# Performance work log

Measured on AMD Instinct MI355X. Metric: run time of the kernel, lower is better.

The kernel has to match this reference:

```python
import jax, jax.numpy as jnp
import numpy as np

B, N, DIM = 4, 1024, 1024
H, DH, ORDER = 16, 64, 3
MAXREL = 64
INNER = H * DH
VOCAB = 2 * MAXREL + 1
SCALE = DH ** -0.5
TOPK = int(0.25 * N)  # topk_ratio=0.25 default when top_k is None


def setup_inputs() -> dict:
    key = jax.random.key(0)
    ks = jax.random.split(key, 8)
    s = 0.02
    return {
        "x": jax.random.normal(ks[0], (B, N, DIM), jnp.float32),
        "Wqkv": jax.random.normal(ks[1], (3 * INNER, DIM), jnp.float32) * s,
        "bqkv": jnp.zeros((3 * INNER,), jnp.float32),
        "Wout": jax.random.normal(ks[2], (DIM, INNER), jnp.float32) * s,
        "bout": jnp.zeros((DIM,), jnp.float32),
        "rel_k_emb": jax.random.normal(ks[3], (VOCAB, DH), jnp.float32) * s,
        "rel_v_emb": jax.random.normal(ks[4], (VOCAB, DH), jnp.float32) * s,
        "alphas_raw": jax.random.normal(ks[5], (ORDER, H), jnp.float32) * 0.5,
    }


def reference(x, Wqkv, bqkv, Wout, bout, rel_k_emb, rel_v_emb, alphas_raw):
    b, n, _ = x.shape
    qkv = x @ Wqkv.T + bqkv  # [b, n, 3*inner]
    q, k, v = jnp.split(qkv, 3, axis=-1)
    to_heads = lambda t: t.reshape(b, n, H, DH).transpose(0, 2, 1, 3)  # b h n d
    q, k, v = to_heads(q), to_heads(k), to_heads(v)

    scores = jnp.einsum('bhid,bhjd->bhij', q, k) * SCALE

    # relative position bias on keys
    coords = jnp.arange(n)
    dist = jnp.clip(coords[:, None] - coords[None, :], -MAXREL, MAXREL) + MAXREL  # [n, n]
    rel_k = rel_k_emb[dist]  # [n, n, d]
    scores = scores + jnp.einsum('bhid,ijd->bhij', q, rel_k)

    # top-k thresholding per query row
    top_vals = jax.lax.top_k(scores, TOPK)[0]
    threshold = top_vals[..., -1:]
    scores = jnp.where(scores < threshold, -jnp.inf, scores)

    attn = jax.nn.softmax(scores, axis=-1)  # [b, h, n, n]

    rel_v = rel_v_emb[dist]  # [n, n, d]
    alphas = jax.nn.sigmoid(alphas_raw)  # [order, h]

    # monomial-basis polynomial filter: res = sum_i alpha_i * A^(i+1) V (+ relV term at i=0)
    res = jnp.zeros_like(v)
    v_curr = v
    for i in range(ORDER):
        a_v = jnp.einsum('bhij,bhjd->bhid', attn, v_curr)
        if i == 0:
            a_v = a_v + jnp.einsum('bhij,ijd->bhid', attn, rel_v)
        v_curr = a_v
        res = res + alphas[i][None, :, None, None] * v_curr

    out = res.transpose(0, 2, 1, 3).reshape(b, n, INNER)
    return out @ Wout.T + bout
```

## Files before the change

kernel.cpp:

```cpp
#include <hip/hip_runtime.h>

typedef unsigned short u16;
typedef unsigned int   u32;
typedef unsigned long long u64;
typedef __bf16 bf16x8 __attribute__((ext_vector_type(8)));
typedef float  floatx4 __attribute__((ext_vector_type(4)));

#define DEV static __device__ __forceinline__

DEV u16 f2bf(float f){ u32 x = __float_as_uint(f); return (u16)((x + 0x7fffu + ((x>>16)&1u)) >> 16); }
DEV float bf2f(u16 h){ return __uint_as_float(((u32)h)<<16); }
DEV u32 cvt_pk_bf16(float a, float b){ u32 r; asm("v_cvt_pk_bf16_f32 %0, %1, %2" : "=v"(r) : "v"(a), "v"(b)); return r; }

DEV void load_lds16(const u16* g, u16* l){
  __builtin_amdgcn_global_load_lds((const __attribute__((address_space(1))) u32*)g,
                                   (__attribute__((address_space(3))) u32*)l, 16, 0, 0);
}

DEV void barrier_fenced(){
  asm volatile("" ::: "memory");
  __builtin_amdgcn_sched_barrier(0);
  __builtin_amdgcn_s_barrier();
  __builtin_amdgcn_sched_barrier(0);
  asm volatile("" ::: "memory");
}

DEV u32 unswz64(u32 p){
  u32 r0 = ((p>>6) ^ (p>>8)) & 1u;
  u32 b4 = ((p>>4) & 1u) ^ r0;
  u32 b5 = ((p>>5) ^ (p>>7)) & 1u;
  return (p & ~0x70u) | (b4<<4) | (b5<<5) | (r0<<6);
}
DEV bf16x8 ldfrag(const u16* base, int row, int lane){
  u32 off = ((u32)row<<6) + (((u32)lane>>4)<<4);
  off ^= (u32)(row&7)<<4;
  return *(const bf16x8*)((const char*)base + off);
}

template<int BM, int BN>
__global__ __launch_bounds__(512, 4) void gemm8(
    const u16* __restrict__ A, const u16* __restrict__ Bm, float* __restrict__ C,
    const float* __restrict__ bias, int K, int lda, int ldb, int ldc, int ncmax)
{
  constexpr int MT = (BM/2)/16;
  constexpr int NT = (BN/4)/16;
  constexpr int AU = BM*32;
  constexpr int BU = BN*32;
  constexpr int STRIDE = AU + BU;
  __shared__ u16 smem[4*STRIDE];

  const int tid = threadIdx.x, wid = tid>>6, lane = tid&63;
  const int m0 = blockIdx.y * BM, n0 = blockIdx.x * BN;

  const u32 g = unswz64((u32)tid*16);
  const int srow = g>>6, schunk = (g&63)>>1;
  const u16* ga0 = A  + (long long)(m0 + srow)*lda + schunk;
  const u16* gb0 = Bm + (long long)(n0 + srow)*ldb + schunk;

  u16* lA0 = smem + (wid<<9);
  u16* lB0 = smem + AU + (wid<<9);

  const int wm = wid>>2, wn = wid&3;
  const int lr = lane&15, lq = lane>>4;

  auto stage = [&](int s){
    const int c = s & 3;
    if (BM == 128 || wid < 4) load_lds16(ga0 + (s<<5), lA0 + c*STRIDE);
    load_lds16(gb0 + (s<<5), lB0 + c*STRIDE);
  };

  floatx4 acc[MT][NT] = {};
  const int nk = K >> 5;

#define G_STEP(CC, VA, VB) do { \
    if (BM == 128 || wid < 4) asm volatile("s_waitcnt vmcnt(" VA ")" ::: "memory"); \
    else                      asm volatile("s_waitcnt vmcnt(" VB ")" ::: "memory"); \
    barrier_fenced(); \
    const u16* Asc = smem + (u32)(CC)*STRIDE; \
    const u16* Bsc = Asc + AU; \
    bf16x8 af[MT]; \
    _Pragma("unroll") \
    for (int mt=0; mt<MT; ++mt) af[mt] = ldfrag(Asc, wm*(BM/2) + mt*16 + lr, lane); \
    _Pragma("unroll") \
    for (int nt=0; nt<NT; ++nt) { \
      bf16x8 bfr = ldfrag(Bsc, wn*(BN/4) + nt*16 + lr, lane); \
      _Pragma("unroll") \
      for (int mt=0; mt<MT; ++mt) \
        acc[mt][nt] = __builtin_amdgcn_mfma_f32_16x16x32_bf16(af[mt], bfr, acc[mt][nt], 0, 0, 0); \
    } \
    barrier_fenced(); \
  } while(0)

#pragma unroll
  for (int p = 0; p < 4; ++p) stage(p);

  for (int s = 0; s < nk - 4; ++s){
    G_STEP(s & 3, "6", "3");
    stage(s + 4);
  }
  G_STEP((nk-4) & 3, "6", "3");
  G_STEP((nk-3) & 3, "4", "2");
  G_STEP((nk-2) & 3, "2", "1");
  G_STEP((nk-1) & 3, "0", "0");
#undef G_STEP

#pragma unroll
  for (int nt=0; nt<NT; ++nt) {
    const int col = n0 + wn*(BN/4) + nt*16 + lr;
    if (col < ncmax) {
      const float bv = bias ? bias[col] : 0.f;
#pragma unroll
      for (int mt=0; mt<MT; ++mt) {
#pragma unroll
        for (int r=0; r<4; ++r) {
          const int row = m0 + wm*(BM/2) + mt*16 + lq*4 + r;
          C[(long long)row*ldc + col] = acc[mt][nt][r] + bv;
        }
      }
    }
  }
}

__global__ __launch_bounds__(512, 4) void av8(
    const u16* __restrict__ P,
    const u16* __restrict__ V,
    u16* __restrict__ vout,
    float* __restrict__ resb,
    const float* __restrict__ araw, int K, int order, int accum, int wv)
{
  __shared__ u16 smem[32768];
  const int tid = threadIdx.x, wid = tid>>6, lane = tid&63;
  const int L = blockIdx.x;
  const int z  = (L & 7) + ((L >> 7) << 3);
  const int m0 = ((L >> 3) & 15) * 64;
  const int lr = lane&15, lq = lane>>4;

  const int sw = wid & 3;
  const u32 g = unswz64((u32)(sw*1024 + lane*16));
  const int srow = g>>6, schunk = (g&63)>>1;
  const u16* gsrc = (wid < 4)
      ? P + (long long)z*1212416 + (long long)(m0 + srow)*1184 + schunk
      : V + (long long)z*75776   + (long long)srow*1184 + schunk;
  const int bsel = (wid < 4) ? 0 : 2048;
  u16* ldst0 = smem + bsel + (sw<<9);

  const int wm = wid>>2, wn = wid&3;
  const int wm32 = wm*32, wn16 = wn*16;
  const int nk = K >> 5;

  auto stage = [&](int p){ load_lds16(gsrc + (p<<5), ldst0 + ((p&7)<<12)); };

  floatx4 acc[2] = {};

#define AV_STEP(CC, VC) do { \
    asm volatile("s_waitcnt vmcnt(" VC ")" ::: "memory"); \
    barrier_fenced(); \
    const u16* Asc = smem + ((u32)(CC)<<12); \
    const u16* Bsc = Asc + 2048; \
    bf16x8 bfr = ldfrag(Bsc, wn16 + lr, lane); \
    bf16x8 af0 = ldfrag(Asc, wm32 + lr, lane); \
    bf16x8 af1 = ldfrag(Asc, wm32 + 16 + lr, lane); \
    acc[0] = __builtin_amdgcn_mfma_f32_16x16x32_bf16(af0, bfr, acc[0], 0, 0, 0); \
    acc[1] = __builtin_amdgcn_mfma_f32_16x16x32_bf16(af1, bfr, acc[1], 0, 0, 0); \
    barrier_fenced(); \
  } while(0)

#pragma unroll
  for (int p = 0; p < 8; ++p) stage(p);

  for (int s = 0; s < nk - 8; ++s){
    AV_STEP(s & 7, "7");
    stage(s + 8);
  }
  AV_STEP((nk-8) & 7, "7");
  AV_STEP((nk-7) & 7, "6");
  AV_STEP((nk-6) & 7, "5");
  AV_STEP((nk-5) & 7, "4");
  AV_STEP((nk-4) & 7, "3");
  AV_STEP((nk-3) & 7, "2");
  AV_STEP((nk-2) & 7, "1");
  AV_STEP((nk-1) & 7, "0");
#undef AV_STEP

  const int h = z & 15;
  const float alpha = 1.f/(1.f + __expf(-araw[order*16 + h]));
  float* rb = resb + (long long)z * 65536;
  const int d = wn16 + lr;
  __syncthreads();
#pragma unroll
  for (int mt=0; mt<2; ++mt){
#pragma unroll
    for (int r=0; r<4; ++r){
      const int row = wm32 + mt*16 + lq*4 + r;
      const float v = acc[mt][r];
      const long long ri = (long long)(m0+row)*64 + d;
      rb[ri] = accum ? (rb[ri] + alpha*v) : (alpha*v);
      smem[d*136 + row] = f2bf(v);
    }
  }
  __syncthreads();
  if (wv){
    const int dd = tid>>3, cc = (tid&7)*8;
    u16* vp = vout + (long long)z*75776 + (long long)dd*1184 + m0 + cc;
    const u16* sp = smem + dd*136 + cc;
    uint4 uu;
    uu.x = sp[0] | ((u32)sp[1]<<16);
    uu.y = sp[2] | ((u32)sp[3]<<16);
    uu.z = sp[4] | ((u32)sp[5]<<16);
    uu.w = sp[6] | ((u32)sp[7]<<16);
    *(uint4*)(vp) = uu;
  }
}

__global__ __launch_bounds__(1024, 8) void score_topk(
    const u16* __restrict__ qF,
    const u16* __restrict__ kxF,
    u16* __restrict__ P)
{
  constexpr int SROW = 1156;
  __shared__ float sm[16*SROW];
  const int tid = threadIdx.x, wid = tid>>6, lane = tid&63;
  const int L = blockIdx.x;
  const int z  = (L & 7) + ((L >> 9) << 3);
  const int mt = (L >> 3) & 63;
  const int m0 = mt*16;
  const int lr = lane&15, lq = lane>>4;

  const u16* Aq = qF + (((long long)z*64 + mt)*6*64 + lane)*8;
  const u16* Bq = kxF + ((long long)z*80*6*64 + lane)*8;

  bf16x8 af[6];
#pragma unroll
  for (int kc=0;kc<6;++kc) af[kc] = *(const bf16x8*)(Aq + kc*512);

  const int base = wid*5;
  {
    floatx4 acc[5];
#pragma unroll
    for (int t=0;t<5;++t) acc[t] = floatx4{0.f,0.f,0.f,0.f};
#pragma unroll
    for (int t=0;t<5;++t){
      if (base + t < 73){
        const u16* bp = Bq + (long long)(base+t)*3072;
        bf16x8 b0 = *(const bf16x8*)(bp);
        bf16x8 b1 = *(const bf16x8*)(bp + 512);
        bf16x8 b2 = *(const bf16x8*)(bp + 1024);
        bf16x8 b3 = *(const bf16x8*)(bp + 1536);
        bf16x8 b4 = *(const bf16x8*)(bp + 2048);
        bf16x8 b5 = *(const bf16x8*)(bp + 2560);
        acc[t] = __builtin_amdgcn_mfma_f32_16x16x32_bf16(af[0], b0, acc[t], 0, 0, 0);
        acc[t] = __builtin_amdgcn_mfma_f32_16x16x32_bf16(af[1], b1, acc[t], 0, 0, 0);
        acc[t] = __builtin_amdgcn_mfma_f32_16x16x32_bf16(af[2], b2, acc[t], 0, 0, 0);
        acc[t] = __builtin_amdgcn_mfma_f32_16x16x32_bf16(af[3], b3, acc[t], 0, 0, 0);
        acc[t] = __builtin_amdgcn_mfma_f32_16x16x32_bf16(af[4], b4, acc[t], 0, 0, 0);
        acc[t] = __builtin_amdgcn_mfma_f32_16x16x32_bf16(af[5], b5, acc[t], 0, 0, 0);
      }
    }
#pragma unroll
    for (int t=0;t<5;++t){
      if (base + t < 73){
        const int col = (base+t)*16 + lr;
        if (col < 1153){
#pragma unroll
          for (int r=0;r<4;++r) sm[(lq*4+r)*SROW + col] = acc[t][r];
        }
      }
    }
  }
  __syncthreads();

  {
    const int row = wid;
    const int i = m0 + row;
    float* R = sm + row*SROW;

    float v[16];
#pragma unroll
    for (int x=0;x<8;++x){
      float2 f = *(const float2*)(R + x*128 + lane*2);
      v[2*x] = f.x; v[2*x+1] = f.y;
    }
#pragma unroll
    for (int x=0;x<16;++x){
      const int j = (x>>1)*128 + lane*2 + (x&1);
      int dl = i - j; dl = dl > 64 ? 64 : (dl < -64 ? -64 : dl);
      v[x] += R[1024 + dl + 64];
    }
    u32 u[16];
#pragma unroll
    for (int x=0;x<16;++x){
      u32 bb = __float_as_uint(v[x]);
      u[x] = bb ^ ((u32)((int)bb >> 31) | 0x80000000u);
    }
    u32 thr = 0;
#pragma unroll 1
    for (int bit=31; bit>=0; --bit){
      const u32 cand = thr | (1u<<bit);
      int c = 0;
#pragma unroll
      for (int x=0;x<16;++x) c += __popcll(__ballot(u[x] >= cand));
      if (c == 256){
        u32 mn = 0xFFFFFFFFu;
#pragma unroll
        for (int x=0;x<16;++x) if (u[x] >= cand && u[x] < mn) mn = u[x];
        for (int o=32;o;o>>=1){ u32 t = __shfl_xor(mn, o); mn = t < mn ? t : mn; }
        thr = mn;
        break;
      }
      if (c > 256) thr = cand;
    }
    float m = -3.0e38f;
#pragma unroll
    for (int x=0;x<16;++x) m = fmaxf(m, v[x]);
    for (int o=32;o;o>>=1) m = fmaxf(m, __shfl_xor(m, o));
    float e[16]; float Z = 0.f;
#pragma unroll
    for (int x=0;x<16;++x){
      e[x] = (u[x] >= thr) ? __expf(v[x]-m) : 0.f;
      Z += e[x];
    }
    for (int o=32;o;o>>=1) Z += __shfl_xor(Z, o);
    const float rz = 1.f / Z;

    u16* Pr = P + ((long long)z*1024 + i)*1184;
    u32* Pr32 = (u32*)Pr;
    float s0 = 0.f, s1 = 0.f;
#pragma unroll
    for (int x=0;x<8;++x){
      const float p0 = e[2*x]*rz, p1 = e[2*x+1]*rz;
      *(float2*)(R + x*128 + lane*2) = float2{p0, p1};
      Pr32[x*64 + lane] = cvt_pk_bf16(p0, p1);
      const int j0 = x*128 + lane*2;
      if (j0     >= i+64) s0 += p0;
      if (j0     <= i-64) s1 += p0;
      if (j0 + 1 >= i+64) s0 += p1;
      if (j0 + 1 <= i-64) s1 += p1;
    }
    for (int o=32;o;o>>=1){ s0 += __shfl_xor(s0,o); s1 += __shfl_xor(s1,o); }
    {
      const int t = lane + 1;
      const int j = i + 64 - t;
      const float wv = (j>=0 && j<1024) ? R[j] : 0.f;
      Pr[1024 + t] = f2bf(wv);
      if (lane < 63){
        const int t2 = lane + 65;
        const int j2 = i + 64 - t2;
        const float wv2 = (j2>=0 && j2<1024) ? R[j2] : 0.f;
        Pr[1024 + t2] = f2bf(wv2);
      }
      if (lane == 0){ Pr[1024] = f2bf(s0); Pr[1152] = f2bf(s1); }
      if (lane >= 33) Pr[1120 + lane] = 0;
    }
  }
}

__global__ __launch_bounds__(256) void planeize(const float* __restrict__ src, u16* __restrict__ dst,
                                                int total, int modeB){
  int idx = blockIdx.x*256 + threadIdx.x;
  if (idx >= total) return;
  int c = idx & 1023, r = idx >> 10;
  float v = src[idx];
  u16 hi = f2bf(v); u16 lo = f2bf(v - bf2f(hi));
  u16* d = dst + (long long)r*3072 + c;
  if (modeB){ d[0]=hi; d[1024]=hi; d[2048]=lo; }
  else      { d[0]=hi; d[1024]=lo; d[2048]=hi; }
}

__global__ __launch_bounds__(256) void build_qk(const float* __restrict__ qkv,
                                                u16* __restrict__ qF, u16* __restrict__ kxF){
  int idx = blockIdx.x*256 + threadIdx.x;
  int d = idx & 63, n = (idx>>6) & 1023, bh = idx >> 16;
  int b = bh >> 4, h = bh & 15;
  long long src = (long long)(b*1024 + n)*3072 + h*64 + d;
  float qv = qkv[src];
  float kv = qkv[src + 1024] * 0.125f;
  u16 qhi=f2bf(qv), qlo=f2bf(qv - bf2f(qhi));
  u16 khi=f2bf(kv), klo=f2bf(kv - bf2f(khi));
  const int lane = (n&15) + (((d&31)>>3)<<4);
  const int elem = d&7, kc0 = d>>5;
  u16* q = qF + ((((long long)bh*64 + (n>>4))*6*64) + lane)*8 + elem;
  q[(kc0+0)*512] = qhi; q[(kc0+2)*512] = qlo; q[(kc0+4)*512] = qhi;
  u16* kx = kxF + ((((long long)bh*80 + (n>>4))*6*64) + lane)*8 + elem;
  kx[(kc0+0)*512] = khi; kx[(kc0+2)*512] = khi; kx[(kc0+4)*512] = klo;
}

__global__ __launch_bounds__(256) void build_kxrel(const float* __restrict__ relk, u16* __restrict__ kxF){
  int idx = blockIdx.x*256 + threadIdx.x;
  int d = idx & 63, t = (idx>>6) & 255, bh = idx >> 14;
  u16 hi=0, lo=0;
  if (t < 129){ float v = relk[t*64 + d]; hi = f2bf(v); lo = f2bf(v - bf2f(hi)); }
  const int nrow = 1024 + t;
  const int lane = (t&15) + (((d&31)>>3)<<4);
  const int elem = d&7, kc0 = d>>5;
  u16* kx = kxF + ((((long long)bh*80 + (nrow>>4))*6*64) + lane)*8 + elem;
  kx[(kc0+0)*512] = hi; kx[(kc0+2)*512] = hi; kx[(kc0+4)*512] = lo;
}

__global__ __launch_bounds__(256) void build_vT(const float* __restrict__ qkv, u16* __restrict__ vA){
  __shared__ float tb[64][65];
  int bh = blockIdx.x >> 4, ntile = blockIdx.x & 15;
  int b = bh >> 4, h = bh & 15;
  int tid = threadIdx.x;
  int nl = tid >> 2, dc = (tid & 3)*16;
  const float* sp = qkv + (long long)(b*1024 + ntile*64 + nl)*3072 + 2048 + h*64 + dc;
#pragma unroll
  for (int j=0;j<16;j+=4){
    float4 f = *(const float4*)(sp + j);
    tb[dc+j+0][nl]=f.x; tb[dc+j+1][nl]=f.y; tb[dc+j+2][nl]=f.z; tb[dc+j+3][nl]=f.w;
  }
  __syncthreads();
  int d = tid >> 2, nc = (tid & 3)*16;
  u16* dp = vA + ((long long)bh*64 + d)*1184 + ntile*64 + nc;
#pragma unroll
  for (int j=0;j<16;j+=8){
    u16 a0=f2bf(tb[d][nc+j+0]), a1=f2bf(tb[d][nc+j+1]), a2=f2bf(tb[d][nc+j+2]), a3=f2bf(tb[d][nc+j+3]);
    u16 a4=f2bf(tb[d][nc+j+4]), a5=f2bf(tb[d][nc+j+5]), a6=f2bf(tb[d][nc+j+6]), a7=f2bf(tb[d][nc+j+7]);
    uint4 uu; uu.x=a0|((u32)a1<<16); uu.y=a2|((u32)a3<<16); uu.z=a4|((u32)a5<<16); uu.w=a6|((u32)a7<<16);
    *(uint4*)(dp + j) = uu;
  }
}

__global__ __launch_bounds__(256) void build_vText(const float* __restrict__ relv, u16* __restrict__ vA){
  int idx = blockIdx.x*256 + threadIdx.x;
  int t = idx % 160; int rest = idx / 160; int d = rest & 63; int bh = rest >> 6;
  u16 hv = 0;
  if (t < 129) hv = f2bf(relv[t*64 + d]);
  vA[((long long)bh*64 + d)*1184 + 1024 + t] = hv;
}

__global__ __launch_bounds__(256) void build_resS(const float* __restrict__ res, u16* __restrict__ resS){
  int idx = blockIdx.x*256 + threadIdx.x;
  int d = idx & 63, n = (idx>>6) & 1023, bh = idx >> 16;
  int b = bh >> 4, h = bh & 15;
  float v = res[idx];
  u16 hi = f2bf(v), lo = f2bf(v - bf2f(hi));
  u16* p = resS + (long long)(b*1024 + n)*3072 + h*64 + d;
  p[0]=hi; p[1024]=lo; p[2048]=hi;
}

extern "C" void kernel_launch(void* const* d_in, const int* in_sizes, int n_in,
                              void* d_out, int out_size, void* d_ws, size_t ws_size,
                              hipStream_t stream) {
  const float* x    = (const float*)d_in[0];
  const float* Wqkv = (const float*)d_in[1];
  const float* bqkv = (const float*)d_in[2];
  const float* Wout = (const float*)d_in[3];
  const float* bout = (const float*)d_in[4];
  const float* relk = (const float*)d_in[5];
  const float* relv = (const float*)d_in[6];
  const float* araw = (const float*)d_in[7];
  float* out = (float*)d_out;

  char* w = (char*)d_ws;
  size_t off = 0;
  auto take = [&](size_t bytes)->char*{ char* p = w + off; off += (bytes + 255) & ~(size_t)255; return p; };

  char* regionA = take(94371840);
  u16*   xS    = (u16*)  (regionA);
  u16*   wqS   = (u16*)  (regionA + 25165824);
  float* qkv32 = (float*)(regionA + 44040192);
  u16*   Ph    = (u16*)  (regionA);
  u16*   resS  = (u16*)  (regionA);
  u16*   woS   = (u16*)  (regionA + 25165824);
  u16*   qF    = (u16*)take(25165824);
  u16*   kxF   = (u16*)take(31457280);
  u16*   vA    = (u16*)take(9699328);
  u16*   vB    = (u16*)take(9699328);
  float* res   = (float*)take(16777216);
  (void)ws_size; (void)in_sizes; (void)n_in; (void)out_size;

  planeize<<<16384,256,0,stream>>>(x,    xS,  4194304, 0);
  planeize<<<12288,256,0,stream>>>(Wqkv, wqS, 3145728, 1);
  gemm8<128,128><<<dim3(16,32,1),512,0,stream>>>(xS, wqS, qkv32, bqkv,
      3072, 3072, 3072, 3072, 2048);
  gemm8<128,128><<<dim3(8,32,1),512,0,stream>>>(xS, wqS + (long long)2048*3072,
      qkv32 + 2048, bqkv + 2048, 1024, 3072, 3072, 3072, 1024);
  build_qk   <<<16384,256,0,stream>>>(qkv32, qF, kxF);
  build_kxrel<<<4096, 256,0,stream>>>(relk, kxF);
  build_vT   <<<1024, 256,0,stream>>>(qkv32, vA);
  build_vText<<<2560, 256,0,stream>>>(relv, vA);

  for (int half = 0; half < 2; ++half) {
    const long long zo = (long long)half * 32;
    score_topk<<<2048,1024,0,stream>>>(qF + zo*196608, kxF + zo*245760, Ph);
    av8<<<512,512,0,stream>>>(Ph, vA + zo*75776, vB + zo*75776, res + zo*65536,
        araw, 1184, 0, 0, 1);
    av8<<<512,512,0,stream>>>(Ph, vB + zo*75776, vA + zo*75776, res + zo*65536,
        araw, 1024, 1, 1, 1);
    av8<<<512,512,0,stream>>>(Ph, vA + zo*75776, vB + zo*75776, res + zo*65536,
        araw, 1024, 2, 1, 0);
  }

  build_resS<<<16384,256,0,stream>>>(res, resS);
  planeize  <<<4096, 256,0,stream>>>(Wout, woS, 1048576, 1);
  gemm8<64,128><<<dim3(8,64,1),512,0,stream>>>(resS, woS, out, bout,
      3072, 3072, 3072, 1024, 1024);
}
```

Before: 538.1 us.

## Double av8 block to 1024 threads with 64-wide K steps and padded rows

The attention-times-V kernel now runs 16 waves per block instead of 8. Each wave computes one 16x16 tile and issues two MFMAs per 64-wide K step. A 4-deep LDS ring replaces the 8-deep one, halving the number of barrier-separated steps. The P and V row strides are padded from 1184 to 1216 so K is a multiple of 64, which adds zero-filling and relocates vB into the reused region A. The trade-off is more threads per block and shallower prefetch against fewer barriers per unit of work.

```diff
diff --git a/kernel.cpp b/kernel.cpp
--- a/kernel.cpp
+++ b/kernel.cpp
@@ -121,7 +121,7 @@
   }
 }
 
-__global__ __launch_bounds__(512, 4) void av8(
+__global__ __launch_bounds__(1024, 8) void av8(
     const u16* __restrict__ P,
     const u16* __restrict__ V,
     u16* __restrict__ vout,
@@ -135,51 +135,47 @@
   const int m0 = ((L >> 3) & 15) * 64;
   const int lr = lane&15, lq = lane>>4;
 
-  const int sw = wid & 3;
+  const int sw = wid & 3, grp = wid >> 2;
   const u32 g = unswz64((u32)(sw*1024 + lane*16));
   const int srow = g>>6, schunk = (g&63)>>1;
-  const u16* gsrc = (wid < 4)
-      ? P + (long long)z*1212416 + (long long)(m0 + srow)*1184 + schunk
-      : V + (long long)z*75776   + (long long)srow*1184 + schunk;
-  const int bsel = (wid < 4) ? 0 : 2048;
-  u16* ldst0 = smem + bsel + (sw<<9);
+  const int koff = (grp & 1) * 32;
+  const u16* gsrc = (grp < 2)
+      ? P + (long long)z*1245184 + (long long)(m0 + srow)*1216 + schunk + koff
+      : V + (long long)z*77824   + (long long)srow*1216 + schunk + koff;
+  u16* ldst0 = smem + grp*2048 + (sw<<9);
 
   const int wm = wid>>2, wn = wid&3;
-  const int wm32 = wm*32, wn16 = wn*16;
-  const int nk = K >> 5;
-
-  auto stage = [&](int p){ load_lds16(gsrc + (p<<5), ldst0 + ((p&7)<<12)); };
-
-  floatx4 acc[2] = {};
+  const int wm16 = wm*16, wn16 = wn*16;
+  const int nk = K >> 6;
+
+  auto stage = [&](int p){ load_lds16(gsrc + (p<<6), ldst0 + ((p&3)<<13)); };
+
+  floatx4 acc = {0.f,0.f,0.f,0.f};
 
 #define AV_STEP(CC, VC) do { \
     asm volatile("s_waitcnt vmcnt(" VC ")" ::: "memory"); \
     barrier_fenced(); \
-    const u16* Asc = smem + ((u32)(CC)<<12); \
-    const u16* Bsc = Asc + 2048; \
-    bf16x8 bfr = ldfrag(Bsc, wn16 + lr, lane); \
-    bf16x8 af0 = ldfrag(Asc, wm32 + lr, lane); \
-    bf16x8 af1 = ldfrag(Asc, wm32 + 16 + lr, lane); \
-    acc[0] = __builtin_amdgcn_mfma_f32_16x16x32_bf16(af0, bfr, acc[0], 0, 0, 0); \
-    acc[1] = __builtin_amdgcn_mfma_f32_16x16x32_bf16(af1, bfr, acc[1], 0, 0, 0); \
+    const u16* bb = smem + ((u32)(CC)<<13); \
+    bf16x8 b0 = ldfrag(bb + 4096, wn16 + lr, lane); \
+    bf16x8 a0 = ldfrag(bb,        wm16 + lr, lane); \
+    acc = __builtin_amdgcn_mfma_f32_16x16x32_bf16(a0, b0, acc, 0, 0, 0); \
+    bf16x8 b1 = ldfrag(bb + 6144, wn16 + lr, lane); \
+    bf16x8 a1 = ldfrag(bb + 2048, wm16 + lr, lane); \
+    acc = __builtin_amdgcn_mfma_f32_16x16x32_bf16(a1, b1, acc, 0, 0, 0); \
     barrier_fenced(); \
   } while(0)
 
 #pragma unroll
-  for (int p = 0; p < 8; ++p) stage(p);
-
-  for (int s = 0; s < nk - 8; ++s){
-    AV_STEP(s & 7, "7");
-    stage(s + 8);
-  }
-  AV_STEP((nk-8) & 7, "7");
-  AV_STEP((nk-7) & 7, "6");
-  AV_STEP((nk-6) & 7, "5");
-  AV_STEP((nk-5) & 7, "4");
-  AV_STEP((nk-4) & 7, "3");
-  AV_STEP((nk-3) & 7, "2");
-  AV_STEP((nk-2) & 7, "1");
-  AV_STEP((nk-1) & 7, "0");
+  for (int p = 0; p < 4; ++p) stage(p);
+
+  for (int s = 0; s < nk - 4; ++s){
+    AV_STEP(s & 3, "3");
+    stage(s + 4);
+  }
+  AV_STEP((nk-4) & 3, "3");
+  AV_STEP((nk-3) & 3, "2");
+  AV_STEP((nk-2) & 3, "1");
+  AV_STEP((nk-1) & 3, "0");
 #undef AV_STEP
 
   const int h = z & 15;
@@ -188,27 +184,22 @@
   const int d = wn16 + lr;
   __syncthreads();
 #pragma unroll
-  for (int mt=0; mt<2; ++mt){
-#pragma unroll
-    for (int r=0; r<4; ++r){
-      const int row = wm32 + mt*16 + lq*4 + r;
-      const float v = acc[mt][r];
-      const long long ri = (long long)(m0+row)*64 + d;
-      rb[ri] = accum ? (rb[ri] + alpha*v) : (alpha*v);
-      smem[d*136 + row] = f2bf(v);
-    }
+  for (int r=0; r<4; ++r){
+    const int row = wm16 + lq*4 + r;
+    const float v = acc[r];
+    const long long ri = (long long)(m0+row)*64 + d;
+    rb[ri] = accum ? (rb[ri] + alpha*v) : (alpha*v);
+    smem[d*136 + row] = f2bf(v);
   }
   __syncthreads();
   if (wv){
-    const int dd = tid>>3, cc = (tid&7)*8;
-    u16* vp = vout + (long long)z*75776 + (long long)dd*1184 + m0 + cc;
+    const int dd = tid>>4, cc = (tid&15)*4;
+    u16* vp = vout + (long long)z*77824 + (long long)dd*1216 + m0 + cc;
     const u16* sp = smem + dd*136 + cc;
-    uint4 uu;
+    uint2 uu;
     uu.x = sp[0] | ((u32)sp[1]<<16);
     uu.y = sp[2] | ((u32)sp[3]<<16);
-    uu.z = sp[4] | ((u32)sp[5]<<16);
-    uu.w = sp[6] | ((u32)sp[7]<<16);
-    *(uint4*)(vp) = uu;
+    *(uint2*)(vp) = uu;
   }
 }
 
@@ -322,7 +313,7 @@
     for (int o=32;o;o>>=1) Z += __shfl_xor(Z, o);
     const float rz = 1.f / Z;
 
-    u16* Pr = P + ((long long)z*1024 + i)*1184;
+    u16* Pr = P + ((long long)z*1024 + i)*1216;
     u32* Pr32 = (u32*)Pr;
     float s0 = 0.f, s1 = 0.f;
 #pragma unroll
@@ -350,6 +341,7 @@
       }
       if (lane == 0){ Pr[1024] = f2bf(s0); Pr[1152] = f2bf(s1); }
       if (lane >= 33) Pr[1120 + lane] = 0;
+      if (lane >= 32) Pr[1152 + lane] = 0;
     }
   }
 }
@@ -410,7 +402,7 @@
   }
   __syncthreads();
   int d = tid >> 2, nc = (tid & 3)*16;
-  u16* dp = vA + ((long long)bh*64 + d)*1184 + ntile*64 + nc;
+  u16* dp = vA + ((long long)bh*64 + d)*1216 + ntile*64 + nc;
 #pragma unroll
   for (int j=0;j<16;j+=8){
     u16 a0=f2bf(tb[d][nc+j+0]), a1=f2bf(tb[d][nc+j+1]), a2=f2bf(tb[d][nc+j+2]), a3=f2bf(tb[d][nc+j+3]);
@@ -422,10 +414,10 @@
 
 __global__ __launch_bounds__(256) void build_vText(const float* __restrict__ relv, u16* __restrict__ vA){
   int idx = blockIdx.x*256 + threadIdx.x;
-  int t = idx % 160; int rest = idx / 160; int d = rest & 63; int bh = rest >> 6;
+  int t = idx % 192; int rest = idx / 192; int d = rest & 63; int bh = rest >> 6;
   u16 hv = 0;
   if (t < 129) hv = f2bf(relv[t*64 + d]);
-  vA[((long long)bh*64 + d)*1184 + 1024 + t] = hv;
+  vA[((long long)bh*64 + d)*1216 + 1024 + t] = hv;
 }
 
 __global__ __launch_bounds__(256) void build_resS(const float* __restrict__ res, u16* __restrict__ resS){
@@ -460,12 +452,12 @@
   u16*   wqS   = (u16*)  (regionA + 25165824);
   float* qkv32 = (float*)(regionA + 44040192);
   u16*   Ph    = (u16*)  (regionA);
+  u16*   vB    = (u16*)  (regionA + 79691776);
   u16*   resS  = (u16*)  (regionA);
   u16*   woS   = (u16*)  (regionA + 25165824);
   u16*   qF    = (u16*)take(25165824);
   u16*   kxF   = (u16*)take(31457280);
-  u16*   vA    = (u16*)take(9699328);
-  u16*   vB    = (u16*)take(9699328);
+  u16*   vA    = (u16*)take(9961472);
   float* res   = (float*)take(16777216);
   (void)ws_size; (void)in_sizes; (void)n_in; (void)out_size;
 
@@ -478,16 +470,16 @@
   build_qk   <<<16384,256,0,stream>>>(qkv32, qF, kxF);
   build_kxrel<<<4096, 256,0,stream>>>(relk, kxF);
   build_vT   <<<1024, 256,0,stream>>>(qkv32, vA);
-  build_vText<<<2560, 256,0,stream>>>(relv, vA);
+  build_vText<<<3072, 256,0,stream>>>(relv, vA);
 
   for (int half = 0; half < 2; ++half) {
     const long long zo = (long long)half * 32;
     score_topk<<<2048,1024,0,stream>>>(qF + zo*196608, kxF + zo*245760, Ph);
-    av8<<<512,512,0,stream>>>(Ph, vA + zo*75776, vB + zo*75776, res + zo*65536,
-        araw, 1184, 0, 0, 1);
-    av8<<<512,512,0,stream>>>(Ph, vB + zo*75776, vA + zo*75776, res + zo*65536,
+    av8<<<512,1024,0,stream>>>(Ph, vA + zo*77824, vB + zo*77824, res + zo*65536,
+        araw, 1216, 0, 0, 1);
+    av8<<<512,1024,0,stream>>>(Ph, vB + zo*77824, vA + zo*77824, res + zo*65536,
         araw, 1024, 1, 1, 1);
-    av8<<<512,512,0,stream>>>(Ph, vA + zo*75776, vB + zo*75776, res + zo*65536,
+    av8<<<512,1024,0,stream>>>(Ph, vA + zo*77824, vB + zo*77824, res + zo*65536,
         araw, 1024, 2, 1, 0);
   }
 
```

After: 539.7 us. Within noise of the previous version (+0.3%).
